# Optimization experiments

Measured on AMD Instinct MI355X. Metric: run time of the kernel, lower is better.

The kernel has to match this reference:

```python
import jax, jax.numpy as jnp
import numpy as np

B, TQ, TK = 2, 2048, 2048
D, H, G = 1024, 16, 4
HD = D // H  # 64
MAX_LEN = 4096


def _rope(x, max_len):
    # x: [B, H, S, hd]; interleaved even/odd RoPE, freqs use full head_dim in denom
    hd = x.shape[-1]
    seq = x.shape[2]
    pos = jnp.arange(max_len, dtype=jnp.float32)[:, None]           # [max_len, 1]
    div = jnp.exp(jnp.arange(0, hd, 2, dtype=jnp.float32) * (-np.log(10000.0) / hd))
    sin = jnp.sin(pos * div)[:seq]                                   # [S, hd/2]
    cos = jnp.cos(pos * div)[:seq]
    xe, xo = x[..., 0::2], x[..., 1::2]
    oe = xe * cos - xo * sin
    oo = xe * sin + xo * cos
    return jnp.stack([oe, oo], axis=-1).reshape(x.shape)


def setup_inputs() -> dict:
    key = jax.random.key(0)
    ks = jax.random.split(key, 10)
    s = 0.02
    return {
        "X": jax.random.normal(ks[0], (B, TQ, D), jnp.float32),
        "encoder_output": jax.random.normal(ks[1], (B, TK, D), jnp.float32),
        "Wq": jax.random.normal(ks[2], (D, D), jnp.float32) * s,
        "bq": jnp.zeros((D,), jnp.float32),
        "Wk": jax.random.normal(ks[3], (D, G * HD), jnp.float32) * s,
        "bk": jnp.zeros((G * HD,), jnp.float32),
        "Wv": jax.random.normal(ks[4], (D, G * HD), jnp.float32) * s,
        "bv": jnp.zeros((G * HD,), jnp.float32),
        "Wo": jax.random.normal(ks[5], (D, D), jnp.float32) * s,
        "bo": jnp.zeros((D,), jnp.float32),
        "max_len": MAX_LEN,
    }


def reference(X, encoder_output, Wq, bq, Wk, bk, Wv, bv, Wo, bo, max_len):
    bsz, tq, d = X.shape
    q = X @ Wq + bq                       # [B, TQ, D]
    k = encoder_output @ Wk + bk          # [B, TK, G*HD]
    v = encoder_output @ Wv + bv

    q = q.reshape(bsz, tq, H, HD).transpose(0, 2, 1, 3)          # [B, H, TQ, HD]
    k = k.reshape(bsz, -1, G, HD).transpose(0, 2, 1, 3)          # [B, G, TK, HD]
    v = v.reshape(bsz, -1, G, HD).transpose(0, 2, 1, 3)
    # expand each group to H//G consecutive heads (matches torch expand+reshape)
    k = jnp.repeat(k, H // G, axis=1)                            # [B, H, TK, HD]
    v = jnp.repeat(v, H // G, axis=1)

    q = _rope(q, max_len)
    k = _rope(k, max_len)

    scores = jnp.einsum("bhqd,bhkd->bhqk", q, k) / jnp.sqrt(jnp.float32(HD))
    w = jax.nn.softmax(scores, axis=-1)
    o = jnp.einsum("bhqk,bhkd->bhqd", w, v)                      # [B, H, TQ, HD]
    o = o.transpose(0, 2, 1, 3).reshape(bsz, tq, d)
    return o @ Wo + bo
```

## Files before the change

### kernel.cpp

```cpp
#include <hip/hip_runtime.h>
#include <cstdint>


typedef __bf16 bf16x8 __attribute__((ext_vector_type(8)));
typedef __bf16 bf16x4v __attribute__((ext_vector_type(4)));
typedef float f32x4 __attribute__((ext_vector_type(4)));

#define MFMA16(a, b, c) __builtin_amdgcn_mfma_f32_16x16x32_bf16((a), (b), (c), 0, 0, 0)

constexpr int Bc = 2, TQc = 2048, TKc = 2048, Dc = 1024, Hc = 16, Gc = 4, HDc = 64;
constexpr float QSCALE = 0.18033688011112042f;

__device__ __forceinline__ ushort bfbits(float x) {
  __bf16 h = (__bf16)x;
  return __builtin_bit_cast(ushort, h);
}

__device__ __forceinline__ float fexp2(float x) {
  float r;
  asm("v_exp_f32 %0, %1" : "=v"(r) : "v"(x));
  return r;
}

__device__ __forceinline__ float fmax3(float a, float b, float c) {
  return fmaxf(fmaxf(a, b), c);
}

__device__ __forceinline__ void async_lds16(void* lds, const void* g) {
  __builtin_amdgcn_global_load_lds((const __attribute__((address_space(1))) uint32_t*)g,
                                   (__attribute__((address_space(3))) uint32_t*)lds,
                                   16, 0, 0);
}

__global__ __launch_bounds__(256) void prep_k(const float* __restrict__ X,
                                              const float* __restrict__ E,
                                              const float* __restrict__ Wq,
                                              const float* __restrict__ Wo,
                                              const float* __restrict__ Wk,
                                              const float* __restrict__ Wv,
                                              ushort* __restrict__ Xb,
                                              ushort* __restrict__ Eb,
                                              ushort* __restrict__ Wqt,
                                              ushort* __restrict__ Wot,
                                              ushort* __restrict__ Wkvt) {
  __shared__ float t[64][65];
  const int bid = blockIdx.x;
  if (bid < 8192) {
    const float* s = (bid < 4096) ? X : E;
    ushort* d = (bid < 4096) ? Xb : Eb;
    int i = (bid & 4095) * 256 + threadIdx.x;
    float4 v = reinterpret_cast<const float4*>(s)[i];
    ushort4 o;
    o.x = bfbits(v.x); o.y = bfbits(v.y); o.z = bfbits(v.z); o.w = bfbits(v.w);
    reinterpret_cast<ushort4*>(d)[i] = o;
    return;
  }
  const int w = bid - 8192;
  const int z = w >> 8, rem = w & 255;
  const int bx = rem & 15, by = rem >> 4;
  const float* src;
  ushort* dst;
  int C, c0;
  if (z == 0)      { src = Wq; dst = Wqt; C = 1024; c0 = bx * 64; }
  else if (z == 1) { src = Wo; dst = Wot; C = 1024; c0 = bx * 64; }
  else {
    if (bx >= 8) return;
    if (bx < 4) { src = Wk; dst = Wkvt; }
    else        { src = Wv; dst = Wkvt + 256 * 1024; }
    C = 256; c0 = (bx & 3) * 64;
  }
  const int r0 = by * 64;
  const int tx = threadIdx.x & 63, ty = threadIdx.x >> 6;
#pragma unroll
  for (int i = 0; i < 16; ++i) {
    int r = i * 4 + ty;
    t[r][tx] = src[(size_t)(r0 + r) * C + c0 + tx];
  }
  __syncthreads();
#pragma unroll
  for (int i = 0; i < 16; ++i) {
    int c = i * 4 + ty;
    dst[(size_t)(c0 + c) * 1024 + r0 + tx] = bfbits(t[tx][c]);
  }
}

__device__ __forceinline__ void gemm_mainloop(const ushort* __restrict__ A,
                                              const ushort* __restrict__ Bt,
                                              int m0, int n0, int K,
                                              char* sA, char* sB,
                                              f32x4 acc[4][2]) {
  const int lane = threadIdx.x & 63, wid = threadIdx.x >> 6;
  const int l15 = lane & 15, l4 = lane >> 4;
  const int wr = (wid >> 1) * 64, wc = (wid & 1) * 32;
  const int srow = lane >> 3;
  const int scc = (lane & 7) ^ (srow & 7);
  const int rxr = l15 & 7;

  const int nsteps = K >> 6;
#pragma unroll
  for (int j = 0; j < 4; ++j) {
    int c = wid * 4 + j;
    async_lds16(sA + c * 1024, A + (size_t)(m0 + c * 8 + srow) * K + scc * 8);
  }
#pragma unroll
  for (int j = 0; j < 2; ++j) {
    int c = wid * 2 + j;
    async_lds16(sB + c * 1024, Bt + (size_t)(n0 + c * 8 + srow) * K + scc * 8);
  }
  __syncthreads();

  int buf = 0;
  for (int s2 = 0; s2 < nsteps; ++s2) {
    if (s2 + 1 < nsteps) {
      const int k0 = (s2 + 1) * 64;
      char* dA = sA + (buf ^ 1) * 16384;
      char* dB = sB + (buf ^ 1) * 8192;
#pragma unroll
      for (int j = 0; j < 4; ++j) {
        int c = wid * 4 + j;
        async_lds16(dA + c * 1024, A + (size_t)(m0 + c * 8 + srow) * K + k0 + scc * 8);
      }
#pragma unroll
      for (int j = 0; j < 2; ++j) {
        int c = wid * 2 + j;
        async_lds16(dB + c * 1024, Bt + (size_t)(n0 + c * 8 + srow) * K + k0 + scc * 8);
      }
    }
    const char* aB = sA + buf * 16384;
    const char* bB = sB + buf * 8192;
    bf16x8 af[2][4], bfr[2][2];
#pragma unroll
    for (int mi = 0; mi < 4; ++mi) {
      const int row = wr + mi * 16 + l15;
#pragma unroll
      for (int kk = 0; kk < 2; ++kk)
        af[kk][mi] = *reinterpret_cast<const bf16x8*>(
            aB + row * 128 + (((l4 + kk * 4) ^ rxr) << 4));
    }
#pragma unroll
    for (int ni = 0; ni < 2; ++ni) {
      const int row = wc + ni * 16 + l15;
#pragma unroll
      for (int kk = 0; kk < 2; ++kk)
        bfr[kk][ni] = *reinterpret_cast<const bf16x8*>(
            bB + row * 128 + (((l4 + kk * 4) ^ rxr) << 4));
    }
#pragma unroll
    for (int kk = 0; kk < 2; ++kk)
#pragma unroll
      for (int mi = 0; mi < 4; ++mi)
#pragma unroll
        for (int ni = 0; ni < 2; ++ni)
          acc[mi][ni] = MFMA16(af[kk][mi], bfr[kk][ni], acc[mi][ni]);
    __syncthreads();
    buf ^= 1;
  }
}

__device__ __forceinline__ void gemm_epilogue(f32x4 acc[4][2], int mode, int m0,
                                              int n0, const float* b0,
                                              const float* b1, float* Cf,
                                              ushort* U0, ushort* U1, int N) {
  const int lane = threadIdx.x & 63, wid = threadIdx.x >> 6;
  const int l15 = lane & 15, l4 = lane >> 4;
  const int wr = (wid >> 1) * 64, wc = (wid & 1) * 32;
#pragma unroll
  for (int ni = 0; ni < 2; ++ni) {
    const int col = n0 + wc + ni * 16 + l15;
    if (mode == 0) {
      const float bv = b0[col];
#pragma unroll
      for (int mi = 0; mi < 4; ++mi) {
        const int rowb = m0 + wr + mi * 16 + l4 * 4;
#pragma unroll
        for (int r = 0; r < 4; ++r)
          Cf[(size_t)(rowb + r) * N + col] = acc[mi][ni][r] + bv;
      }
    } else if (mode == 1) {
      const int h = col >> 6, d = col & 63, fi = d >> 1, odd = d & 1;
      const float div = __expf(-0.28782313662425572f * (float)fi);
      const float bv = b0[col];
#pragma unroll
      for (int mi = 0; mi < 4; ++mi) {
        const int rowb = m0 + wr + mi * 16 + l4 * 4;
#pragma unroll
        for (int r = 0; r < 4; ++r) {
          const int row = rowb + r, b = row >> 11, t = row & 2047;
          const float val = acc[mi][ni][r] + bv;
          const float prt = __shfl_xor(val, 1);
          float sn, cs;
          __sincosf((float)t * div, &sn, &cs);
          const float o = odd ? (prt * sn + val * cs) : (val * cs - prt * sn);
          U0[(((size_t)(b * Hc + h)) * TQc + t) * HDc + d] = bfbits(o * QSCALE);
        }
      }
    } else {
      if (col < 256) {
        const int g = col >> 6, d = col & 63, fi = d >> 1, odd = d & 1;
        const float div = __expf(-0.28782313662425572f * (float)fi);
        const float bv = b0[col];
#pragma unroll
        for (int mi = 0; mi < 4; ++mi) {
          const int rowb = m0 + wr + mi * 16 + l4 * 4;
#pragma unroll
          for (int r = 0; r < 4; ++r) {
            const int row = rowb + r, b = row >> 11, t = row & 2047;
            const float val = acc[mi][ni][r] + bv;
            const float prt = __shfl_xor(val, 1);
            float sn, cs;
            __sincosf((float)t * div, &sn, &cs);
            const float o = odd ? (prt * sn + val * cs) : (val * cs - prt * sn);
            U0[(((size_t)(b * Gc + g)) * TKc + t) * HDc + d] = bfbits(o);
          }
        }
      } else {
        const int c2 = col - 256;
        const int g = c2 >> 6, d = c2 & 63;
        const float bv = b1[c2];
#pragma unroll
        for (int mi = 0; mi < 4; ++mi) {
          const int rowb = m0 + wr + mi * 16 + l4 * 4;
          const int b = rowb >> 11, t0 = rowb & 2047;
          ushort4 w;
          w.x = bfbits(acc[mi][ni][0] + bv);
          w.y = bfbits(acc[mi][ni][1] + bv);
          w.z = bfbits(acc[mi][ni][2] + bv);
          w.w = bfbits(acc[mi][ni][3] + bv);
          *reinterpret_cast<ushort4*>(
              &U1[(((size_t)(b * Gc + g)) * HDc + d) * TKc + t0]) = w;
        }
      }
    }
  }
}

__global__ __launch_bounds__(256) void qkv_k(const ushort* __restrict__ Xb,
                                             const ushort* __restrict__ Eb,
                                             const ushort* __restrict__ Wqt,
                                             const ushort* __restrict__ Wkvt,
                                             const float* __restrict__ bq,
                                             const float* __restrict__ bk,
                                             const float* __restrict__ bv,
                                             ushort* __restrict__ Qb,
                                             ushort* __restrict__ Kb,
                                             ushort* __restrict__ Vt) {
  __shared__ __attribute__((aligned(16))) char smem[48 * 1024];
  const int bid = blockIdx.x;
  const ushort *A, *Bt;
  const float *b0, *b1 = nullptr;
  ushort *U0, *U1 = nullptr;
  int mode, tb, tn;
  if (bid < 512) { A = Xb; Bt = Wqt; b0 = bq; U0 = Qb; mode = 1; tb = bid; tn = 16; }
  else { A = Eb; Bt = Wkvt; b0 = bk; b1 = bv; U0 = Kb; U1 = Vt; mode = 2; tb = bid - 512; tn = 8; }
  const int m0 = (tb / tn) * 128, n0 = (tb % tn) * 64;
  const f32x4 z = {0.f, 0.f, 0.f, 0.f};
  f32x4 acc[4][2] = {{z, z}, {z, z}, {z, z}, {z, z}};
  gemm_mainloop(A, Bt, m0, n0, 1024, smem, smem + 32768, acc);
  gemm_epilogue(acc, mode, m0, n0, b0, b1, nullptr, U0, U1, 0);
}

__global__ __launch_bounds__(256) void oproj_k(const ushort* __restrict__ Ob,
                                               const ushort* __restrict__ Wot,
                                               const float* __restrict__ bo,
                                               float* __restrict__ out) {
  __shared__ __attribute__((aligned(16))) char smem[48 * 1024];
  const int bid = blockIdx.x;
  const int m0 = (bid >> 4) * 128, n0 = (bid & 15) * 64;
  const f32x4 z = {0.f, 0.f, 0.f, 0.f};
  f32x4 acc[4][2] = {{z, z}, {z, z}, {z, z}, {z, z}};
  gemm_mainloop(Ob, Wot, m0, n0, 1024, smem, smem + 32768, acc);
  gemm_epilogue(acc, 0, m0, n0, bo, nullptr, out, nullptr, nullptr, 1024);
}

__global__ __launch_bounds__(512, 4) void attn_k(const ushort* __restrict__ Qg,
                                                 const ushort* __restrict__ Kg,
                                                 const ushort* __restrict__ Vg,
                                                 ushort* __restrict__ Ob) {
  __shared__ __attribute__((aligned(16))) char smem[64 * 1024];
  const int lane = threadIdx.x & 63, wid = threadIdx.x >> 6;
  const int l15 = lane & 15, l4 = lane >> 4;
  const int bid = blockIdx.x;
  const int bg = bid & 7, pos = bid >> 3;
  const int b = bg >> 2, g = bg & 3;
  const int h = g * 4 + (pos >> 4);
  const int q0 = (pos & 15) * 128 + wid * 16;
  const ushort* Qp = Qg + ((size_t)(b * Hc + h)) * TQc * HDc;
  const ushort* Kp = Kg + ((size_t)(b * Gc + g)) * TKc * HDc;
  const ushort* Vp = Vg + ((size_t)(b * Gc + g)) * HDc * TKc;
  char* k0 = smem;
  char* k1 = smem + 8192;
  char* k2 = smem + 16384;
  char* v0 = smem + 24576;
  char* v1 = smem + 32768;
  char* v2 = smem + 40960;
  char* pb = smem + 49152 + wid * 2048;
  const int rx = (l15 & 7) << 4;
  const int swz = l15 & 7;

  const int sr = wid * 8 + (lane >> 3);
  const int sc = (lane & 7) ^ ((lane >> 3) & 7);
  const char* KstN = (const char*)Kp + (size_t)sr * 128 + sc * 16;
  const char* VstN = (const char*)Vp + (size_t)sr * (TKc * 2) + sc * 16;

  bf16x8 bq0 = *reinterpret_cast<const bf16x8*>(Qp + (size_t)(q0 + l15) * HDc + l4 * 8);
  bf16x8 bq1 = *reinterpret_cast<const bf16x8*>(Qp + (size_t)(q0 + l15) * HDc + 32 + l4 * 8);

  bf16x8 vones;
#pragma unroll
  for (int i = 0; i < 8; ++i) vones[i] = (__bf16)1.0f;

  float m = -INFINITY;
  const f32x4 z = {0.f, 0.f, 0.f, 0.f};
  f32x4 accO[4] = {z, z, z, z};
  f32x4 acc1 = z;

  constexpr int NT = TKc / 64;
  async_lds16(k0 + wid * 1024, KstN);
  async_lds16(v0 + wid * 1024, VstN);
  KstN += 8192; VstN += 128;
  async_lds16(k1 + wid * 1024, KstN);
  async_lds16(v1 + wid * 1024, VstN);
  KstN += 8192; VstN += 128;

  for (int kt = 0; kt < NT; ++kt) {
    if (kt < NT - 1) asm volatile("s_waitcnt vmcnt(2)" ::: "memory");
    else             asm volatile("s_waitcnt vmcnt(0)" ::: "memory");
    __builtin_amdgcn_s_barrier();
    __builtin_amdgcn_sched_barrier(0);
    if (kt + 2 < NT) {
      async_lds16(k2 + wid * 1024, KstN);
      async_lds16(v2 + wid * 1024, VstN);
      KstN += 8192; VstN += 128;
    }

    f32x4 s[4] = {z, z, z, z};
#pragma unroll
    for (int nf = 0; nf < 4; ++nf) {
      const char* krow = k0 + (nf * 16 + l15) * 128;
      bf16x8 kf0 = *reinterpret_cast<const bf16x8*>(krow + ((l4 ^ swz) << 4));
      bf16x8 kf1 = *reinterpret_cast<const bf16x8*>(krow + (((4 + l4) ^ swz) << 4));
      s[nf] = MFMA16(kf0, bq0, s[nf]);
      s[nf] = MFMA16(kf1, bq1, s[nf]);
    }
    bf16x8 va[4][2];
#pragma unroll
    for (int df = 0; df < 4; ++df) {
      const char* vrow = v0 + (df * 16 + l15) * 128;
      va[df][0] = *reinterpret_cast<const bf16x8*>(vrow + ((l4 ^ swz) << 4));
      va[df][1] = *reinterpret_cast<const bf16x8*>(vrow + (((4 + l4) ^ swz) << 4));
    }

    float pm = fmax3(fmax3(s[0][0], s[0][1], s[0][2]),
                     fmax3(s[0][3], s[1][0], s[1][1]),
                     fmax3(s[1][2], s[1][3], s[2][0]));
    pm = fmax3(pm,
               fmax3(s[2][1], s[2][2], s[2][3]),
               fmax3(s[3][0], s[3][1], fmaxf(s[3][2], s[3][3])));
    pm = fmaxf(pm, __shfl_xor(pm, 16));
    pm = fmaxf(pm, __shfl_xor(pm, 32));
    if (!__all(pm - m <= 11.5f)) {
      float mn = fmaxf(m, pm);
      float sc2 = fexp2(m - mn);
      m = mn;
      acc1 *= sc2;
#pragma unroll
      for (int df = 0; df < 4; ++df) accO[df] *= sc2;
    }
#pragma unroll
    for (int nf = 0; nf < 4; ++nf)
#pragma unroll
      for (int r = 0; r < 4; ++r)
        s[nf][r] = fexp2(s[nf][r] - m);

#pragma unroll
    for (int nf = 0; nf < 4; ++nf) {
      bf16x4v pv;
      pv[0] = (__bf16)s[nf][0];
      pv[1] = (__bf16)s[nf][1];
      pv[2] = (__bf16)s[nf][2];
      pv[3] = (__bf16)s[nf][3];
      *reinterpret_cast<uint2*>(pb + l15 * 128 + ((nf * 32 + l4 * 8) ^ rx)) =
          __builtin_bit_cast(uint2, pv);
    }
    asm volatile("" ::: "memory");
    bf16x8 ap0 = *reinterpret_cast<const bf16x8*>(pb + l15 * 128 + ((l4 * 16) ^ rx));
    bf16x8 ap1 = *reinterpret_cast<const bf16x8*>(pb + l15 * 128 + ((64 + l4 * 16) ^ rx));
#pragma unroll
    for (int df = 0; df < 4; ++df)
      accO[df] = MFMA16(ap1, va[df][1], MFMA16(ap0, va[df][0], accO[df]));
    acc1 = MFMA16(ap1, vones, MFMA16(ap0, vones, acc1));

    char* tk = k0; k0 = k1; k1 = k2; k2 = tk;
    char* tv = v0; v0 = v1; v1 = v2; v2 = tv;
  }

  float inv[4];
#pragma unroll
  for (int r = 0; r < 4; ++r) inv[r] = 1.f / acc1[r];
#pragma unroll
  for (int df = 0; df < 4; ++df)
#pragma unroll
    for (int r = 0; r < 4; ++r) {
      int row = q0 + l4 * 4 + r;
      int col = h * HDc + df * 16 + l15;
      Ob[((size_t)b * TQc + row) * Dc + col] = bfbits(accO[df][r] * inv[r]);
    }
}

extern "C" void kernel_launch(void* const* d_in, const int* in_sizes, int n_in,
                              void* d_out, int out_size, void* d_ws, size_t ws_size,
                              hipStream_t stream) {
  const float* X  = (const float*)d_in[0];
  const float* E  = (const float*)d_in[1];
  const float* Wq = (const float*)d_in[2];
  const float* bq = (const float*)d_in[3];
  const float* Wk = (const float*)d_in[4];
  const float* bk = (const float*)d_in[5];
  const float* Wv = (const float*)d_in[6];
  const float* bv = (const float*)d_in[7];
  const float* Wo = (const float*)d_in[8];
  const float* bo = (const float*)d_in[9];
  float* out = (float*)d_out;
  char* ws = (char*)d_ws;

  const size_t MB = 1ull << 20;
  if (ws_size < 42 * MB) return;

  ushort* Xb   = (ushort*)(ws + 0 * MB);
  ushort* Eb   = (ushort*)(ws + 8 * MB);
  ushort* Wqt  = (ushort*)(ws + 16 * MB);
  ushort* Wkvt = (ushort*)(ws + 18 * MB);
  ushort* Wot  = (ushort*)(ws + 19 * MB);
  ushort* Qb   = (ushort*)(ws + 21 * MB);
  ushort* Kb   = (ushort*)(ws + 29 * MB);
  ushort* Vt   = (ushort*)(ws + 31 * MB);
  ushort* Ob   = (ushort*)(ws + 33 * MB);

  prep_k<<<dim3(8960), 256, 0, stream>>>(X, E, Wq, Wo, Wk, Wv, Xb, Eb, Wqt, Wot, Wkvt);
  qkv_k<<<dim3(768), 256, 0, stream>>>(Xb, Eb, Wqt, Wkvt, bq, bk, bv, Qb, Kb, Vt);
  attn_k<<<dim3(512), dim3(512), 0, stream>>>(Qb, Kb, Vt, Ob);
  oproj_k<<<dim3(512), 256, 0, stream>>>(Ob, Wot, bo, out);
}
```

Measured before the change: 103.7 us.

## Double attention block size and switch K/V staging to double buffering

```diff
diff --git a/kernel.cpp b/kernel.cpp
--- a/kernel.cpp
+++ b/kernel.cpp
@@ -272,35 +272,35 @@
   gemm_epilogue(acc, 0, m0, n0, bo, nullptr, out, nullptr, nullptr, 1024);
 }
 
-__global__ __launch_bounds__(512, 4) void attn_k(const ushort* __restrict__ Qg,
-                                                 const ushort* __restrict__ Kg,
-                                                 const ushort* __restrict__ Vg,
-                                                 ushort* __restrict__ Ob) {
+__global__ __launch_bounds__(1024, 4) void attn_k(const ushort* __restrict__ Qg,
+                                                  const ushort* __restrict__ Kg,
+                                                  const ushort* __restrict__ Vg,
+                                                  ushort* __restrict__ Ob) {
   __shared__ __attribute__((aligned(16))) char smem[64 * 1024];
   const int lane = threadIdx.x & 63, wid = threadIdx.x >> 6;
   const int l15 = lane & 15, l4 = lane >> 4;
   const int bid = blockIdx.x;
   const int bg = bid & 7, pos = bid >> 3;
   const int b = bg >> 2, g = bg & 3;
-  const int h = g * 4 + (pos >> 4);
-  const int q0 = (pos & 15) * 128 + wid * 16;
+  const int h = g * 4 + (pos >> 3);
+  const int q0 = (pos & 7) * 256 + wid * 16;
   const ushort* Qp = Qg + ((size_t)(b * Hc + h)) * TQc * HDc;
   const ushort* Kp = Kg + ((size_t)(b * Gc + g)) * TKc * HDc;
   const ushort* Vp = Vg + ((size_t)(b * Gc + g)) * HDc * TKc;
-  char* k0 = smem;
-  char* k1 = smem + 8192;
-  char* k2 = smem + 16384;
-  char* v0 = smem + 24576;
-  char* v1 = smem + 32768;
-  char* v2 = smem + 40960;
-  char* pb = smem + 49152 + wid * 2048;
+  char* sK = smem;
+  char* sV = smem + 16384;
+  char* pb = smem + 32768 + wid * 2048;
   const int rx = (l15 & 7) << 4;
   const int swz = l15 & 7;
 
-  const int sr = wid * 8 + (lane >> 3);
+  const int wkv = wid & 7;
+  const int sr = wkv * 8 + (lane >> 3);
   const int sc = (lane & 7) ^ ((lane >> 3) & 7);
-  const char* KstN = (const char*)Kp + (size_t)sr * 128 + sc * 16;
-  const char* VstN = (const char*)Vp + (size_t)sr * (TKc * 2) + sc * 16;
+  const bool isK = (wid < 8);
+  const char* srcN = isK ? (const char*)Kp + (size_t)sr * 128 + sc * 16
+                         : (const char*)Vp + (size_t)sr * (TKc * 2) + sc * 16;
+  const size_t srcStep = isK ? 8192 : 128;
+  char* dstBase = (isK ? sK : sV) + wkv * 1024;
 
   bf16x8 bq0 = *reinterpret_cast<const bf16x8*>(Qp + (size_t)(q0 + l15) * HDc + l4 * 8);
   bf16x8 bq1 = *reinterpret_cast<const bf16x8*>(Qp + (size_t)(q0 + l15) * HDc + 32 + l4 * 8);
@@ -315,28 +315,23 @@
   f32x4 acc1 = z;
 
   constexpr int NT = TKc / 64;
-  async_lds16(k0 + wid * 1024, KstN);
-  async_lds16(v0 + wid * 1024, VstN);
-  KstN += 8192; VstN += 128;
-  async_lds16(k1 + wid * 1024, KstN);
-  async_lds16(v1 + wid * 1024, VstN);
-  KstN += 8192; VstN += 128;
-
+  async_lds16(dstBase, srcN);
+  srcN += srcStep;
+  __syncthreads();
+
+  int buf = 0;
   for (int kt = 0; kt < NT; ++kt) {
-    if (kt < NT - 1) asm volatile("s_waitcnt vmcnt(2)" ::: "memory");
-    else             asm volatile("s_waitcnt vmcnt(0)" ::: "memory");
-    __builtin_amdgcn_s_barrier();
-    __builtin_amdgcn_sched_barrier(0);
-    if (kt + 2 < NT) {
-      async_lds16(k2 + wid * 1024, KstN);
-      async_lds16(v2 + wid * 1024, VstN);
-      KstN += 8192; VstN += 128;
-    }
+    if (kt + 1 < NT) {
+      async_lds16(dstBase + (buf ^ 1) * 8192, srcN);
+      srcN += srcStep;
+    }
+    const char* sKb = sK + buf * 8192;
+    const char* sVb = sV + buf * 8192;
 
     f32x4 s[4] = {z, z, z, z};
 #pragma unroll
     for (int nf = 0; nf < 4; ++nf) {
-      const char* krow = k0 + (nf * 16 + l15) * 128;
+      const char* krow = sKb + (nf * 16 + l15) * 128;
       bf16x8 kf0 = *reinterpret_cast<const bf16x8*>(krow + ((l4 ^ swz) << 4));
       bf16x8 kf1 = *reinterpret_cast<const bf16x8*>(krow + (((4 + l4) ^ swz) << 4));
       s[nf] = MFMA16(kf0, bq0, s[nf]);
@@ -345,7 +340,7 @@
     bf16x8 va[4][2];
 #pragma unroll
     for (int df = 0; df < 4; ++df) {
-      const char* vrow = v0 + (df * 16 + l15) * 128;
+      const char* vrow = sVb + (df * 16 + l15) * 128;
       va[df][0] = *reinterpret_cast<const bf16x8*>(vrow + ((l4 ^ swz) << 4));
       va[df][1] = *reinterpret_cast<const bf16x8*>(vrow + (((4 + l4) ^ swz) << 4));
     }
@@ -390,8 +385,8 @@
       accO[df] = MFMA16(ap1, va[df][1], MFMA16(ap0, va[df][0], accO[df]));
     acc1 = MFMA16(ap1, vones, MFMA16(ap0, vones, acc1));
 
-    char* tk = k0; k0 = k1; k1 = k2; k2 = tk;
-    char* tv = v0; v0 = v1; v1 = v2; v2 = tv;
+    __syncthreads();
+    buf ^= 1;
   }
 
   float inv[4];
@@ -438,6 +433,6 @@
 
   prep_k<<<dim3(8960), 256, 0, stream>>>(X, E, Wq, Wo, Wk, Wv, Xb, Eb, Wqt, Wot, Wkvt);
   qkv_k<<<dim3(768), 256, 0, stream>>>(Xb, Eb, Wqt, Wkvt, bq, bk, bv, Qb, Kb, Vt);
-  attn_k<<<dim3(512), dim3(512), 0, stream>>>(Qb, Kb, Vt, Ob);
+  attn_k<<<dim3(256), dim3(1024), 0, stream>>>(Qb, Kb, Vt, Ob);
   oproj_k<<<dim3(512), 256, 0, stream>>>(Ob, Wot, bo, out);
 }
```

After: 100.2 us. 1.03x faster.
